# Performance work log

Measured on AMD Instinct MI355X. Metric: run time of the kernel, lower is better.

Reference implementation:

```python
import jax, jax.numpy as jnp
import numpy as np

N_NODES = 100000
N_EDGES = 3200000
N_FEAT = 128
HIDDEN = 64
N_CLASSES = 3
N_GRAPHS = 512
BN_EPS = 1e-5


def setup_inputs() -> dict:
    key = jax.random.key(0)
    ks = jax.random.split(key, 16)
    x = jax.random.normal(ks[0], (N_NODES, N_FEAT), dtype=jnp.float32)
    edge_index = jax.random.randint(ks[1], (2, N_EDGES), 0, N_NODES, dtype=jnp.int64)
    batch = jnp.sort(jax.random.randint(ks[2], (N_NODES,), 0, N_GRAPHS, dtype=jnp.int64))
    # GCNConv weights (glorot-ish scale), biases
    W1 = jax.random.normal(ks[3], (N_FEAT, HIDDEN), dtype=jnp.float32) / np.sqrt(N_FEAT)
    b1 = jnp.zeros((HIDDEN,), dtype=jnp.float32)
    W2 = jax.random.normal(ks[4], (HIDDEN, HIDDEN), dtype=jnp.float32) / np.sqrt(HIDDEN)
    b2 = jnp.zeros((HIDDEN,), dtype=jnp.float32)
    # BatchNorm params + running stats (eval mode)
    g1 = jnp.ones((HIDDEN,), dtype=jnp.float32)
    bt1 = jnp.zeros((HIDDEN,), dtype=jnp.float32)
    rm1 = jax.random.normal(ks[5], (HIDDEN,), dtype=jnp.float32) * 0.1
    rv1 = jax.random.uniform(ks[6], (HIDDEN,), dtype=jnp.float32) + 0.5
    g2 = jnp.ones((HIDDEN,), dtype=jnp.float32)
    bt2 = jnp.zeros((HIDDEN,), dtype=jnp.float32)
    rm2 = jax.random.normal(ks[7], (HIDDEN,), dtype=jnp.float32) * 0.1
    rv2 = jax.random.uniform(ks[8], (HIDDEN,), dtype=jnp.float32) + 0.5
    # classifier
    Wc = jax.random.normal(ks[9], (HIDDEN, N_CLASSES), dtype=jnp.float32) / np.sqrt(HIDDEN)
    bc = jnp.zeros((N_CLASSES,), dtype=jnp.float32)
    return dict(x=x, W1=W1, b1=b1, g1=g1, bt1=bt1, rm1=rm1, rv1=rv1,
                W2=W2, b2=b2, g2=g2, bt2=bt2, rm2=rm2, rv2=rv2,
                Wc=Wc, bc=bc, edge_index=edge_index, batch=batch)


def _gcn_conv(x, W, b, src, dst):
    # x' = D^{-1/2} (A + I) D^{-1/2} X W + b  (PyG GCNConv with self-loops)
    n = x.shape[0]
    h = x @ W  # [N, H]
    loops = jnp.arange(n, dtype=src.dtype)
    s = jnp.concatenate([src, loops])
    d = jnp.concatenate([dst, loops])
    deg = jax.ops.segment_sum(jnp.ones_like(d, dtype=h.dtype), d, num_segments=n)
    dinv = jnp.where(deg > 0, jax.lax.rsqrt(deg), 0.0)
    norm = dinv[s] * dinv[d]  # [E+N]
    msg = h[s] * norm[:, None]  # gather + scale
    out = jax.ops.segment_sum(msg, d, num_segments=n)  # scatter-add
    return out + b


def _bn_eval(x, gamma, beta, rmean, rvar):
    return (x - rmean) * jax.lax.rsqrt(rvar + BN_EPS) * gamma + beta


def reference(x, W1, b1, g1, bt1, rm1, rv1, W2, b2, g2, bt2, rm2, rv2, Wc, bc, edge_index, batch):
    src, dst = edge_index[0], edge_index[1]
    h = _gcn_conv(x, W1, b1, src, dst)
    h = jax.nn.relu(_bn_eval(h, g1, bt1, rm1, rv1))
    # dropout inactive in eval mode
    h = _gcn_conv(h, W2, b2, src, dst)
    h = jax.nn.relu(_bn_eval(h, g2, bt2, rm2, rv2))
    # global mean pool over graphs
    sums = jax.ops.segment_sum(h, batch, num_segments=N_GRAPHS)
    cnts = jax.ops.segment_sum(jnp.ones((h.shape[0],), dtype=h.dtype), batch, num_segments=N_GRAPHS)
    pooled = sums / jnp.maximum(cnts, 1.0)[:, None]  # [G, H]
    return pooled @ Wc + bc  # [G, C]
```

## Files before the change

### kernel.cpp

```cpp
#include <hip/hip_runtime.h>

#define NN 100000
#define NE 3200000
#define NG 512
#define NCB 391
#define BN_EPS 1e-5f

typedef unsigned short u16;
typedef unsigned int u32;

__device__ __forceinline__ u16 f2bf(float f) {
    u32 u = __float_as_uint(f);
    u += 0x7FFF + ((u >> 16) & 1);
    return (u16)(u >> 16);
}

__global__ __launch_bounds__(256) void k_chist(const int* __restrict__ dst, int* __restrict__ ccount) {
    __shared__ int h[NCB];
    int t = threadIdx.x;
    for (int i = t; i < NCB; i += 256) h[i] = 0;
    __syncthreads();
    int stride = gridDim.x * 256;
    for (int e = blockIdx.x * 256 + t; e < NE; e += stride)
        atomicAdd(&h[dst[e] >> 8], 1);
    __syncthreads();
    for (int i = t; i < NCB; i += 256)
        if (h[i]) atomicAdd(&ccount[i], h[i]);
}

__global__ __launch_bounds__(256) void k_cscan(const int* __restrict__ ccount, int* __restrict__ cbase,
                                               int* __restrict__ fbase, int* __restrict__ gcur) {
    __shared__ int sh[256], sh2[256];
    int t = threadIdx.x;
    int v[2], w[2];
    int s = 0, s2 = 0;
#pragma unroll
    for (int j = 0; j < 2; j++) {
        int idx = t * 2 + j;
        int c = (idx < NCB) ? ccount[idx] : 0;
        v[j] = c;
        w[j] = (idx < NCB) ? ((c + 771) & ~3) : 0;
        s += v[j]; s2 += w[j];
    }
    sh[t] = s; sh2[t] = s2;
    __syncthreads();
    for (int off = 1; off < 256; off <<= 1) {
        int x = (t >= off) ? sh[t - off] : 0;
        int x2 = (t >= off) ? sh2[t - off] : 0;
        __syncthreads();
        sh[t] += x; sh2[t] += x2;
        __syncthreads();
    }
    int run = sh[t] - s, run2 = sh2[t] - s2;
#pragma unroll
    for (int j = 0; j < 2; j++) {
        int idx = t * 2 + j;
        if (idx < NCB) { cbase[idx] = run; gcur[idx] = run; fbase[idx] = run2; }
        run += v[j]; run2 += w[j];
    }
    if (t == 255) cbase[NCB] = run;
}

#define P1_CHUNK 8192
__global__ __launch_bounds__(1024) void k_p1(const int* __restrict__ src, const int* __restrict__ dst,
                                             int* __restrict__ gcur, int* __restrict__ esc) {
    __shared__ int ccur[NCB];
    __shared__ int lstart[NCB];
    __shared__ int gbase[NCB];
    __shared__ int sc[512];
    __shared__ int lbuf[P1_CHUNK];
    __shared__ u16 lbkt[P1_CHUNK];
    const int t = threadIdx.x;
    const int e0 = blockIdx.x * P1_CHUNK;
    if (t < NCB) ccur[t] = 0;
    __syncthreads();
    int n = NE - e0; if (n > P1_CHUNK) n = P1_CHUNK;
    for (int idx = t; idx < n; idx += 1024)
        atomicAdd(&ccur[dst[e0 + idx] >> 8], 1);
    __syncthreads();
    int cnt = 0;
    if (t < 512) { cnt = (t < NCB) ? ccur[t] : 0; sc[t] = cnt; }
    __syncthreads();
    for (int off = 1; off < 512; off <<= 1) {
        int x = (t >= off && t < 512) ? sc[t - off] : 0;
        __syncthreads();
        if (t < 512) sc[t] += x;
        __syncthreads();
    }
    if (t < NCB) {
        int ls = sc[t] - cnt;
        lstart[t] = ls;
        ccur[t] = ls;
        gbase[t] = (cnt > 0) ? atomicAdd(&gcur[t], cnt) : 0;
    }
    __syncthreads();
    for (int idx = t; idx < n; idx += 1024) {
        int dd = dst[e0 + idx];
        int s = src[e0 + idx];
        int b = dd >> 8;
        int pos = atomicAdd(&ccur[b], 1);
        lbuf[pos] = s | ((dd & 255) << 17);
        lbkt[pos] = (u16)b;
    }
    __syncthreads();
    for (int p = t; p < n; p += 1024) {
        int b = lbkt[p];
        esc[gbase[b] + (p - lstart[b])] = lbuf[p];
    }
}

__global__ __launch_bounds__(256) void k_p2(const int* __restrict__ esc, const int* __restrict__ cbase,
                                            const int* __restrict__ fbase, int* __restrict__ esf,
                                            int* __restrict__ offs, int* __restrict__ cntp,
                                            float* __restrict__ dinv) {
    __shared__ int lcnt[256], sh[256], lcur[256];
    int t = threadIdx.x, b = blockIdx.x;
    int c0 = cbase[b], c1 = cbase[b + 1];
    lcnt[t] = 0;
    __syncthreads();
    for (int i = c0 + t; i < c1; i += 256) atomicAdd(&lcnt[esc[i] >> 17], 1);
    __syncthreads();
    int cnt = lcnt[t];
    int p = (cnt + 3) & ~3;
    sh[t] = p;
    __syncthreads();
    for (int off = 1; off < 256; off <<= 1) {
        int x = (t >= off) ? sh[t - off] : 0;
        __syncthreads();
        sh[t] += x;
        __syncthreads();
    }
    int fb = fbase[b];
    int o = fb + sh[t] - p;
    lcur[t] = o;
    int node = (b << 8) + t;
    if (node < NN) {
        offs[node] = o;
        cntp[node] = p;
        dinv[node] = rsqrtf((float)(cnt + 1));
        for (int q = cnt; q < p; q++) esf[o + q] = NN;
    }
    __syncthreads();
    for (int i = c0 + t; i < c1; i += 256) {
        int rec = esc[i];
        int pos = atomicAdd(&lcur[rec >> 17], 1);
        esf[pos] = rec & 0x1FFFF;
    }
}

template <int K>
__global__ __launch_bounds__(256) void k_gemm(const float* __restrict__ X,
                                              const float* __restrict__ W,
                                              const float* __restrict__ dinv,
                                              u16* __restrict__ hp, int M) {
    __shared__ float ws[K * 64];
    const int t = threadIdx.x;
    const int row0 = blockIdx.x * 128;
    const int rg = t >> 3;
    const int f0 = (t & 7) * 8;

    const float4* Wg = (const float4*)W;
    float4* ws4 = (float4*)ws;
#pragma unroll
    for (int i = 0; i < (K * 16) / 256; i++) ws4[t + i * 256] = Wg[t + i * 256];
    __syncthreads();

    float acc[4][8];
#pragma unroll
    for (int j = 0; j < 4; j++)
#pragma unroll
        for (int c = 0; c < 8; c++) acc[j][c] = 0.0f;

    const float* xr[4];
#pragma unroll
    for (int j = 0; j < 4; j++) {
        int row = row0 + rg + 32 * j;
        xr[j] = X + (size_t)(row < M ? row : 0) * K;
    }

#pragma unroll 2
    for (int kk = 0; kk < K; kk += 4) {
        float4 xv[4];
#pragma unroll
        for (int j = 0; j < 4; j++) xv[j] = *(const float4*)(xr[j] + kk);
#pragma unroll
        for (int kki = 0; kki < 4; kki++) {
            float4 w0 = *(const float4*)(&ws[(kk + kki) * 64 + f0]);
            float4 w1 = *(const float4*)(&ws[(kk + kki) * 64 + f0 + 4]);
#pragma unroll
            for (int j = 0; j < 4; j++) {
                float a = (&xv[j].x)[kki];
                acc[j][0] = fmaf(a, w0.x, acc[j][0]);
                acc[j][1] = fmaf(a, w0.y, acc[j][1]);
                acc[j][2] = fmaf(a, w0.z, acc[j][2]);
                acc[j][3] = fmaf(a, w0.w, acc[j][3]);
                acc[j][4] = fmaf(a, w1.x, acc[j][4]);
                acc[j][5] = fmaf(a, w1.y, acc[j][5]);
                acc[j][6] = fmaf(a, w1.z, acc[j][6]);
                acc[j][7] = fmaf(a, w1.w, acc[j][7]);
            }
        }
    }

#pragma unroll
    for (int j = 0; j < 4; j++) {
        int row = row0 + rg + 32 * j;
        if (row < M) {
            float di = dinv[row];
            uint4 pk;
            pk.x = (u32)f2bf(acc[j][0] * di) | ((u32)f2bf(acc[j][1] * di) << 16);
            pk.y = (u32)f2bf(acc[j][2] * di) | ((u32)f2bf(acc[j][3] * di) << 16);
            pk.z = (u32)f2bf(acc[j][4] * di) | ((u32)f2bf(acc[j][5] * di) << 16);
            pk.w = (u32)f2bf(acc[j][6] * di) | ((u32)f2bf(acc[j][7] * di) << 16);
            *(uint4*)(hp + (size_t)row * 64 + f0) = pk;
        }
    }
}

__global__ __launch_bounds__(256) void k_agg(const u32* __restrict__ hp2,
                                             const int* __restrict__ esf,
                                             const int* __restrict__ offs,
                                             const int* __restrict__ cntp,
                                             const float* __restrict__ dinv,
                                             const float* __restrict__ bias,
                                             const float* __restrict__ gam,
                                             const float* __restrict__ bet,
                                             const float* __restrict__ rm,
                                             const float* __restrict__ rv,
                                             float* __restrict__ out) {
    const int lane = threadIdx.x & 63;
    const int half = lane >> 5;
    const int fp = lane & 31;
    const int node = (blockIdx.x * 256 + threadIdx.x) >> 6;
    if (node >= NN) return;
    const int beg = offs[node];
    const int mp = cntp[node];
    float ax = 0.0f, ay = 0.0f;
    for (int c = 0; c < mp; c += 64) {
        int m = mp - c;
        if (m > 64) m = 64;
        int rec = (lane < m) ? esf[beg + c + lane] : NN;
        int j = 0;
        for (; j + 16 <= m; j += 16) {
            u32 v[8];
#pragma unroll
            for (int u = 0; u < 8; u++) {
                int s = __shfl(rec, j + 2 * u + half);
                v[u] = hp2[(size_t)s * 32 + fp];
            }
#pragma unroll
            for (int u = 0; u < 8; u++) {
                ax += __uint_as_float(v[u] << 16);
                ay += __uint_as_float(v[u] & 0xFFFF0000u);
            }
        }
        for (; j < m; j += 4) {
            int s0 = __shfl(rec, j + half);
            int s1 = __shfl(rec, j + 2 + half);
            u32 v0 = hp2[(size_t)s0 * 32 + fp];
            u32 v1 = hp2[(size_t)s1 * 32 + fp];
            ax += __uint_as_float(v0 << 16);
            ay += __uint_as_float(v0 & 0xFFFF0000u);
            ax += __uint_as_float(v1 << 16);
            ay += __uint_as_float(v1 & 0xFFFF0000u);
        }
    }
    ax += __shfl_xor(ax, 32);
    ay += __shfl_xor(ay, 32);
    u32 sv = hp2[(size_t)node * 32 + fp];
    ax += __uint_as_float(sv << 16);
    ay += __uint_as_float(sv & 0xFFFF0000u);

    const float di = dinv[node];
    const int f0 = fp * 2;
    float2 bia = *(const float2*)(bias + f0);
    float2 ga  = *(const float2*)(gam + f0);
    float2 be  = *(const float2*)(bet + f0);
    float2 rme = *(const float2*)(rm + f0);
    float2 rva = *(const float2*)(rv + f0);
    float vx = ax * di + bia.x;
    float vy = ay * di + bia.y;
    float yx = (vx - rme.x) * (ga.x * rsqrtf(rva.x + BN_EPS)) + be.x;
    float yy = (vy - rme.y) * (ga.y * rsqrtf(rva.y + BN_EPS)) + be.y;
    if (half == 0)
        *(float2*)(out + (size_t)node * 64 + f0) = make_float2(fmaxf(yx, 0.0f), fmaxf(yy, 0.0f));
}

__global__ __launch_bounds__(256) void k_poolcls(const float* __restrict__ h,
                                                 const int* __restrict__ batch,
                                                 const float* __restrict__ Wc,
                                                 const float* __restrict__ bc,
                                                 float* __restrict__ out) {
    __shared__ float sh[256];
    const int g = blockIdx.x;
    const int t = threadIdx.x;
    const int lane = t & 63;
    const int wv = t >> 6;
    int lo = 0, hi = NN;
    while (lo < hi) { int mid = (lo + hi) >> 1; if (batch[mid] < g) lo = mid + 1; else hi = mid; }
    const int r0 = lo;
    hi = NN;
    while (lo < hi) { int mid = (lo + hi) >> 1; if (batch[mid] < g + 1) lo = mid + 1; else hi = mid; }
    const int r1 = lo;
    float acc = 0.0f;
    for (int r = r0 + wv; r < r1; r += 4)
        acc += h[(size_t)r * 64 + lane];
    sh[t] = acc;
    __syncthreads();
    if (wv == 0) {
        float p = sh[lane] + sh[64 + lane] + sh[128 + lane] + sh[192 + lane];
        p *= 1.0f / fmaxf((float)(r1 - r0), 1.0f);
        float c0 = p * Wc[lane * 3 + 0];
        float c1 = p * Wc[lane * 3 + 1];
        float c2 = p * Wc[lane * 3 + 2];
        for (int o = 32; o > 0; o >>= 1) {
            c0 += __shfl_xor(c0, o);
            c1 += __shfl_xor(c1, o);
            c2 += __shfl_xor(c2, o);
        }
        if (lane == 0) {
            out[g * 3 + 0] = c0 + bc[0];
            out[g * 3 + 1] = c1 + bc[1];
            out[g * 3 + 2] = c2 + bc[2];
        }
    }
}

extern "C" void kernel_launch(void* const* d_in, const int* in_sizes, int n_in,
                              void* d_out, int out_size, void* d_ws, size_t ws_size,
                              hipStream_t stream) {
    const float* x   = (const float*)d_in[0];
    const float* W1  = (const float*)d_in[1];
    const float* b1  = (const float*)d_in[2];
    const float* g1  = (const float*)d_in[3];
    const float* bt1 = (const float*)d_in[4];
    const float* rm1 = (const float*)d_in[5];
    const float* rv1 = (const float*)d_in[6];
    const float* W2  = (const float*)d_in[7];
    const float* b2  = (const float*)d_in[8];
    const float* g2  = (const float*)d_in[9];
    const float* bt2 = (const float*)d_in[10];
    const float* rm2 = (const float*)d_in[11];
    const float* rv2 = (const float*)d_in[12];
    const float* Wc  = (const float*)d_in[13];
    const float* bc  = (const float*)d_in[14];
    const int* ei    = (const int*)d_in[15];
    const int* batch = (const int*)d_in[16];
    const int* srcp = ei;
    const int* dstp = ei + NE;

    char* ws = (char*)d_ws;
    u16*   hpb    = (u16*)(ws);
    int*   ccount = (int*)(ws + 12800128);
    int*   cbase  = (int*)(ws + 12803264);
    int*   fbase  = (int*)(ws + 12806400);
    int*   gcur   = (int*)(ws + 12809536);
    int*   offs   = (int*)(ws + 12812672);
    int*   cntp   = (int*)(ws + 13212672);
    float* dinv   = (float*)(ws + 13612672);
    int*   esf    = (int*)(ws + 14012672);
    float* bufB   = (float*)(ws + 28052672);
    int*   esc    = (int*)(ws + 28052672);

    hipMemsetAsync(hpb + (size_t)NN * 64, 0, 128 + NCB * 4, stream);

    k_chist<<<512, 256, 0, stream>>>(dstp, ccount);
    k_cscan<<<1, 256, 0, stream>>>(ccount, cbase, fbase, gcur);
    k_p1<<<(NE + P1_CHUNK - 1) / P1_CHUNK, 1024, 0, stream>>>(srcp, dstp, gcur, esc);
    k_p2<<<NCB, 256, 0, stream>>>(esc, cbase, fbase, esf, offs, cntp, dinv);

    k_gemm<128><<<(NN + 127) / 128, 256, 0, stream>>>(x, W1, dinv, hpb, NN);
    k_agg<<<(NN * 64 + 255) / 256, 256, 0, stream>>>((const u32*)hpb, esf, offs, cntp, dinv, b1, g1, bt1, rm1, rv1, bufB);

    k_gemm<64><<<(NN + 127) / 128, 256, 0, stream>>>(bufB, W2, dinv, hpb, NN);
    k_agg<<<(NN * 64 + 255) / 256, 256, 0, stream>>>((const u32*)hpb, esf, offs, cntp, dinv, b2, g2, bt2, rm2, rv2, bufB);

    k_poolcls<<<NG, 256, 0, stream>>>(bufB, batch, Wc, bc, (float*)d_out);
}
```

Before: 384.0 us.

## Replace histogram and scan pre-pass with fixed-capacity coarse buckets

Removes the coarse histogram kernel and the single-block scan. Each coarse bucket now gets a fixed slot of C_BKT entries, and its running atomic counter doubles as the bucket's edge count. This saves a full pass over the destination indices plus two launches and their serialization. It also drops the padding of per-node edge lists to multiples of four and the NN sentinel fill. The risks are that any bucket holding more than C_BKT edges would overflow into its neighbour, and that the aggregation kernel may assume padded neighbour counts.

```diff
diff --git a/kernel.cpp b/kernel.cpp
--- a/kernel.cpp
+++ b/kernel.cpp
@@ -4,6 +4,7 @@
 #define NE 3200000
 #define NG 512
 #define NCB 391
+#define C_BKT 8912
 #define BN_EPS 1e-5f
 
 typedef unsigned short u16;
@@ -15,55 +16,9 @@
     return (u16)(u >> 16);
 }
 
-__global__ __launch_bounds__(256) void k_chist(const int* __restrict__ dst, int* __restrict__ ccount) {
-    __shared__ int h[NCB];
-    int t = threadIdx.x;
-    for (int i = t; i < NCB; i += 256) h[i] = 0;
-    __syncthreads();
-    int stride = gridDim.x * 256;
-    for (int e = blockIdx.x * 256 + t; e < NE; e += stride)
-        atomicAdd(&h[dst[e] >> 8], 1);
-    __syncthreads();
-    for (int i = t; i < NCB; i += 256)
-        if (h[i]) atomicAdd(&ccount[i], h[i]);
-}
-
-__global__ __launch_bounds__(256) void k_cscan(const int* __restrict__ ccount, int* __restrict__ cbase,
-                                               int* __restrict__ fbase, int* __restrict__ gcur) {
-    __shared__ int sh[256], sh2[256];
-    int t = threadIdx.x;
-    int v[2], w[2];
-    int s = 0, s2 = 0;
-#pragma unroll
-    for (int j = 0; j < 2; j++) {
-        int idx = t * 2 + j;
-        int c = (idx < NCB) ? ccount[idx] : 0;
-        v[j] = c;
-        w[j] = (idx < NCB) ? ((c + 771) & ~3) : 0;
-        s += v[j]; s2 += w[j];
-    }
-    sh[t] = s; sh2[t] = s2;
-    __syncthreads();
-    for (int off = 1; off < 256; off <<= 1) {
-        int x = (t >= off) ? sh[t - off] : 0;
-        int x2 = (t >= off) ? sh2[t - off] : 0;
-        __syncthreads();
-        sh[t] += x; sh2[t] += x2;
-        __syncthreads();
-    }
-    int run = sh[t] - s, run2 = sh2[t] - s2;
-#pragma unroll
-    for (int j = 0; j < 2; j++) {
-        int idx = t * 2 + j;
-        if (idx < NCB) { cbase[idx] = run; gcur[idx] = run; fbase[idx] = run2; }
-        run += v[j]; run2 += w[j];
-    }
-    if (t == 255) cbase[NCB] = run;
-}
-
 #define P1_CHUNK 8192
 __global__ __launch_bounds__(1024) void k_p1(const int* __restrict__ src, const int* __restrict__ dst,
-                                             int* __restrict__ gcur, int* __restrict__ esc) {
+                                             int* __restrict__ gcur0, int* __restrict__ esc) {
     __shared__ int ccur[NCB];
     __shared__ int lstart[NCB];
     __shared__ int gbase[NCB];
@@ -91,7 +46,7 @@
         int ls = sc[t] - cnt;
         lstart[t] = ls;
         ccur[t] = ls;
-        gbase[t] = (cnt > 0) ? atomicAdd(&gcur[t], cnt) : 0;
+        gbase[t] = (cnt > 0) ? (t * C_BKT + atomicAdd(&gcur0[t], cnt)) : 0;
     }
     __syncthreads();
     for (int idx = t; idx < n; idx += 1024) {
@@ -109,20 +64,20 @@
     }
 }
 
-__global__ __launch_bounds__(256) void k_p2(const int* __restrict__ esc, const int* __restrict__ cbase,
-                                            const int* __restrict__ fbase, int* __restrict__ esf,
+__global__ __launch_bounds__(256) void k_p2(const int* __restrict__ esc, const int* __restrict__ gcur0,
+                                            int* __restrict__ esf,
                                             int* __restrict__ offs, int* __restrict__ cntp,
                                             float* __restrict__ dinv) {
     __shared__ int lcnt[256], sh[256], lcur[256];
     int t = threadIdx.x, b = blockIdx.x;
-    int c0 = cbase[b], c1 = cbase[b + 1];
+    int c0 = b * C_BKT;
+    int c1 = c0 + gcur0[b];
     lcnt[t] = 0;
     __syncthreads();
     for (int i = c0 + t; i < c1; i += 256) atomicAdd(&lcnt[esc[i] >> 17], 1);
     __syncthreads();
     int cnt = lcnt[t];
-    int p = (cnt + 3) & ~3;
-    sh[t] = p;
+    sh[t] = cnt;
     __syncthreads();
     for (int off = 1; off < 256; off <<= 1) {
         int x = (t >= off) ? sh[t - off] : 0;
@@ -130,15 +85,13 @@
         sh[t] += x;
         __syncthreads();
     }
-    int fb = fbase[b];
-    int o = fb + sh[t] - p;
+    int o = c0 + sh[t] - cnt;
     lcur[t] = o;
     int node = (b << 8) + t;
     if (node < NN) {
         offs[node] = o;
-        cntp[node] = p;
+        cntp[node] = cnt;
         dinv[node] = rsqrtf((float)(cnt + 1));
-        for (int q = cnt; q < p; q++) esf[o + q] = NN;
     }
     __syncthreads();
     for (int i = c0 + t; i < c1; i += 256) {
@@ -351,10 +304,7 @@
 
     char* ws = (char*)d_ws;
     u16*   hpb    = (u16*)(ws);
-    int*   ccount = (int*)(ws + 12800128);
-    int*   cbase  = (int*)(ws + 12803264);
-    int*   fbase  = (int*)(ws + 12806400);
-    int*   gcur   = (int*)(ws + 12809536);
+    int*   gcur0  = (int*)(ws + 12800128);
     int*   offs   = (int*)(ws + 12812672);
     int*   cntp   = (int*)(ws + 13212672);
     float* dinv   = (float*)(ws + 13612672);
@@ -364,10 +314,8 @@
 
     hipMemsetAsync(hpb + (size_t)NN * 64, 0, 128 + NCB * 4, stream);
 
-    k_chist<<<512, 256, 0, stream>>>(dstp, ccount);
-    k_cscan<<<1, 256, 0, stream>>>(ccount, cbase, fbase, gcur);
-    k_p1<<<(NE + P1_CHUNK - 1) / P1_CHUNK, 1024, 0, stream>>>(srcp, dstp, gcur, esc);
-    k_p2<<<NCB, 256, 0, stream>>>(esc, cbase, fbase, esf, offs, cntp, dinv);
+    k_p1<<<(NE + P1_CHUNK - 1) / P1_CHUNK, 1024, 0, stream>>>(srcp, dstp, gcur0, esc);
+    k_p2<<<NCB, 256, 0, stream>>>(esc, gcur0, esf, offs, cntp, dinv);
 
     k_gemm<128><<<(NN + 127) / 128, 256, 0, stream>>>(x, W1, dinv, hpb, NN);
     k_agg<<<(NN * 64 + 255) / 256, 256, 0, stream>>>((const u32*)hpb, esf, offs, cntp, dinv, b1, g1, bt1, rm1, rv1, bufB);
```

Measured after the change: 365.8 us. -4.8%, faster.
